# Performance work log

Measured on AMD Instinct MI355X. Metric: run time of the kernel, lower is better.

The kernel has to match this reference:

```python
import jax, jax.numpy as jnp
import numpy as np

B, S, H, NH = 2, 2048, 2048, 32
HD = H // NH  # 64

def _causal_mask(b, s, dtype=jnp.float32):
    neg = jnp.finfo(dtype).min
    m = jnp.where(jnp.tril(jnp.ones((s, s), dtype=bool)), 0.0, neg).astype(dtype)
    return jnp.broadcast_to(m[None, None], (b, 1, s, s))

def setup_inputs() -> dict:
    key = jax.random.key(0)
    k1, k2, k3, k4, k5 = jax.random.split(key, 5)
    scale = 1.0 / np.sqrt(H)
    return {
        "hidden_states": jax.random.normal(k1, (B, S, H), jnp.float32),
        "attention_mask": _causal_mask(B, S),
        "Wq": jax.random.normal(k2, (H, H), jnp.float32) * scale,
        "Wk": jax.random.normal(k3, (H, H), jnp.float32) * scale,
        "Wv": jax.random.normal(k4, (H, H), jnp.float32) * scale,
        "Wo": jax.random.normal(k5, (H, H), jnp.float32) * scale,
    }

def reference(hidden_states, attention_mask, Wq, Wk, Wv, Wo):
    b, s, _ = hidden_states.shape
    dt = hidden_states.dtype
    def proj(W):  # torch Linear: x @ W.T -> [b, nh, s, hd]
        return (hidden_states @ W.T).reshape(b, s, NH, HD).transpose(0, 2, 1, 3)
    q, k, v = proj(Wq), proj(Wk), proj(Wv)
    attn = jnp.einsum('bhqd,bhkd->bhqk', q, k) / np.sqrt(HD)
    attn = attn + attention_mask
    attn = jnp.maximum(attn, jnp.finfo(attn.dtype).min)
    attn = jax.nn.softmax(attn.astype(jnp.float32), axis=-1).astype(dt)
    out = jnp.einsum('bhqk,bhkd->bhqd', attn, v)
    out = out.transpose(0, 2, 1, 3).reshape(b, s, H)
    return out @ Wo.T
```

## Files before the change

kernel.cpp:

```cpp
#include <hip/hip_runtime.h>
#include <hip/hip_bf16.h>
#include <stdint.h>

#define S_LEN 2048
#define NHEAD 32
#define HDIM  64

using bf16x8 = __attribute__((ext_vector_type(8))) short;
using f32x4  = __attribute__((ext_vector_type(4))) float;
using f32x16 = __attribute__((ext_vector_type(16))) float;

__device__ __forceinline__ uint16_t f2bf(float f) {
  union { float f; uint32_t u; } c; c.f = f;
  uint32_t u = c.u;
  return (uint16_t)((u + 0x7FFFu + ((u >> 16) & 1u)) >> 16);
}

__device__ __forceinline__ void load_lds16(const void* g, void* l) {
  __builtin_amdgcn_global_load_lds(
      (const __attribute__((address_space(1))) void*)g,
      (__attribute__((address_space(3))) void*)l, 16, 0, 0);
}

__device__ __forceinline__ f32x16 mfma32(bf16x8 a, bf16x8 b, f32x16 c) {
  return __builtin_amdgcn_mfma_f32_32x32x16_bf16(a, b, c, 0, 0, 0);
}

__device__ __forceinline__ uint32_t cvtpk(float lo, float hi_) {
  uint32_t d;
  asm("v_cvt_pk_bf16_f32 %0, %1, %2" : "=v"(d) : "v"(lo), "v"(hi_));
  return d;
}
__device__ __forceinline__ void plswap(uint32_t& a, uint32_t& b) {
  asm volatile("v_permlane32_swap_b32 %0, %1" : "+v"(a), "+v"(b));
}
__device__ __forceinline__ float exp2_hw(float x) {
  float r;
  asm("v_exp_f32 %0, %1" : "=v"(r) : "v"(x));
  return r;
}

__global__ __launch_bounds__(256) void conv_batch(
    const float* __restrict__ X, const float* __restrict__ Wq,
    const float* __restrict__ Wk, const float* __restrict__ Wv,
    const float* __restrict__ Wo, uint16_t* __restrict__ Xbf,
    uint16_t* __restrict__ Wqk, uint16_t* __restrict__ Wvb,
    uint16_t* __restrict__ Wob) {
  int i = blockIdx.x * 256 + threadIdx.x;
  const float* src; uint16_t* dst; int o;
  if (i < 2097152)      { src = X;  dst = Xbf;           o = i; }
  else if (i < 3145728) { src = Wq; dst = Wqk;           o = i - 2097152; }
  else if (i < 4194304) { src = Wk; dst = Wqk + 4194304; o = i - 3145728; }
  else if (i < 5242880) { src = Wv; dst = Wvb;           o = i - 4194304; }
  else                  { src = Wo; dst = Wob;           o = i - 5242880; }
  float4 v = ((const float4*)src)[o];
  uint64_t packed = (uint64_t)f2bf(v.x) | ((uint64_t)f2bf(v.y) << 16) |
                    ((uint64_t)f2bf(v.z) << 32) | ((uint64_t)f2bf(v.w) << 48);
  ((uint64_t*)dst)[o] = packed;
}

__global__ __launch_bounds__(512, 2) void gemm_qk(
    const uint16_t* __restrict__ A, const uint16_t* __restrict__ Bw,
    uint16_t* __restrict__ Qo, uint16_t* __restrict__ Ko, float qscale) {
  extern __shared__ char smem[];
  const int t = threadIdx.x;
  const int lane = t & 63, w = t >> 6;
  const int lrow = lane & 15, lgrp = lane >> 4;
  const int wr = w >> 2, wc = w & 3;
  const int id = blockIdx.x;
  const int swz = (id & 7) * 32 + (id >> 3);
  const int bm = (swz & 15) * 256, bn = (swz >> 4) * 256;
  constexpr int NT = 2048 / 64;

  const f32x4 zero4 = {0.f, 0.f, 0.f, 0.f};
  f32x4 acc[8][4];
#pragma unroll
  for (int mi = 0; mi < 8; ++mi)
#pragma unroll
    for (int ni = 0; ni < 4; ++ni) acc[mi][ni] = zero4;

  auto stage_half = [&](const uint16_t* __restrict__ G, int grow0,
                        char* dstHalf, int kt) {
#pragma unroll
    for (int j = 0; j < 2; ++j) {
      const int s = t + j * 512;
      const int lr = s >> 3;
      const int sc = (s & 7) ^ (lr & 7);
      load_lds16(G + (size_t)(grow0 + lr) * 2048 + kt * 64 + sc * 8,
                 dstHalf + j * 8192 + w * 1024);
    }
  };
  auto ldA = [&](const char* bufA, int mh, int mi2, int kk) -> bf16x8 {
    const int lr = mh * 64 + mi2 * 16 + lrow;
    const int c = kk * 4 + lgrp;
    return *(const bf16x8*)(bufA + wr * 16384 + lr * 128 +
                            ((c ^ (lr & 7)) << 4));
  };
  auto ldB = [&](const char* bufB, int nh, int ni2, int kk) -> bf16x8 {
    const int lr = (wc & 1) * 64 + nh * 32 + ni2 * 16 + lrow;
    const int c = kk * 4 + lgrp;
    return *(const bf16x8*)(bufB + (wc >> 1) * 16384 + lr * 128 +
                            ((c ^ (lr & 7)) << 4));
  };

  stage_half(A, bm, smem, 0);
  stage_half(A, bm + 128, smem + 16384, 0);
  stage_half(Bw, bn, smem + 32768, 0);
  stage_half(Bw, bn + 128, smem + 49152, 0);

  for (int kt = 0; kt < NT; ++kt) {
    char* bufc = smem + (kt & 1) * 65536;
    char* bufn = smem + ((kt + 1) & 1) * 65536;
    const char* Ac = bufc;
    const char* Bc = bufc + 32768;
    const bool pre = (kt + 1 < NT);

    asm volatile("s_waitcnt vmcnt(0)" ::: "memory");
    __builtin_amdgcn_s_barrier();

    bf16x8 aF[4][2], b0[2][2], b1[2][2];

#pragma unroll
    for (int mi2 = 0; mi2 < 4; ++mi2)
#pragma unroll
      for (int kk = 0; kk < 2; ++kk) aF[mi2][kk] = ldA(Ac, 0, mi2, kk);
#pragma unroll
    for (int ni2 = 0; ni2 < 2; ++ni2)
#pragma unroll
      for (int kk = 0; kk < 2; ++kk) b0[ni2][kk] = ldB(Bc, 0, ni2, kk);
    if (pre) stage_half(A, bm, bufn, kt + 1);
    asm volatile("s_waitcnt lgkmcnt(0)" ::: "memory");
    __builtin_amdgcn_sched_barrier(0);
    __builtin_amdgcn_s_setprio(1);
#pragma unroll
    for (int mi2 = 0; mi2 < 4; ++mi2)
#pragma unroll
      for (int ni2 = 0; ni2 < 2; ++ni2)
#pragma unroll
        for (int kk = 0; kk < 2; ++kk)
          acc[mi2][ni2] = __builtin_amdgcn_mfma_f32_16x16x32_bf16(
              aF[mi2][kk], b0[ni2][kk], acc[mi2][ni2], 0, 0, 0);
    __builtin_amdgcn_s_setprio(0);

#pragma unroll
    for (int ni2 = 0; ni2 < 2; ++ni2)
#pragma unroll
      for (int kk = 0; kk < 2; ++kk) b1[ni2][kk] = ldB(Bc, 1, ni2, kk);
    if (pre) stage_half(A, bm + 128, bufn + 16384, kt + 1);
    asm volatile("s_waitcnt lgkmcnt(0)" ::: "memory");
    __builtin_amdgcn_sched_barrier(0);
    __builtin_amdgcn_s_setprio(1);
#pragma unroll
    for (int mi2 = 0; mi2 < 4; ++mi2)
#pragma unroll
      for (int ni2 = 0; ni2 < 2; ++ni2)
#pragma unroll
        for (int kk = 0; kk < 2; ++kk)
          acc[mi2][2 + ni2] = __builtin_amdgcn_mfma_f32_16x16x32_bf16(
              aF[mi2][kk], b1[ni2][kk], acc[mi2][2 + ni2], 0, 0, 0);
    __builtin_amdgcn_s_setprio(0);

#pragma unroll
    for (int mi2 = 0; mi2 < 4; ++mi2)
#pragma unroll
      for (int kk = 0; kk < 2; ++kk) aF[mi2][kk] = ldA(Ac, 1, mi2, kk);
    if (pre) stage_half(Bw, bn, bufn + 32768, kt + 1);
    asm volatile("s_waitcnt lgkmcnt(0)" ::: "memory");
    __builtin_amdgcn_sched_barrier(0);
    __builtin_amdgcn_s_setprio(1);
#pragma unroll
    for (int mi2 = 0; mi2 < 4; ++mi2)
#pragma unroll
      for (int ni2 = 0; ni2 < 2; ++ni2)
#pragma unroll
        for (int kk = 0; kk < 2; ++kk)
          acc[4 + mi2][2 + ni2] = __builtin_amdgcn_mfma_f32_16x16x32_bf16(
              aF[mi2][kk], b1[ni2][kk], acc[4 + mi2][2 + ni2], 0, 0, 0);
    __builtin_amdgcn_s_setprio(0);

    if (pre) stage_half(Bw, bn + 128, bufn + 49152, kt + 1);
    __builtin_amdgcn_s_setprio(1);
#pragma unroll
    for (int mi2 = 0; mi2 < 4; ++mi2)
#pragma unroll
      for (int ni2 = 0; ni2 < 2; ++ni2)
#pragma unroll
        for (int kk = 0; kk < 2; ++kk)
          acc[4 + mi2][ni2] = __builtin_amdgcn_mfma_f32_16x16x32_bf16(
              aF[mi2][kk], b0[ni2][kk], acc[4 + mi2][ni2], 0, 0, 0);
    __builtin_amdgcn_s_setprio(0);
  }

  const bool isQ = (bn < 2048);
#pragma unroll
  for (int mi = 0; mi < 8; ++mi) {
#pragma unroll
    for (int ni = 0; ni < 4; ++ni) {
      const int n = bn + wc * 64 + ni * 16 + lrow;
      const int n2 = isQ ? n : (n - 2048);
      const int h = n2 >> 6, d = n2 & 63;
#pragma unroll
      for (int r = 0; r < 4; ++r) {
        const int m = bm + wr * 128 + mi * 16 + lgrp * 4 + r;
        const int b = m >> 11, s = m & 2047;
        const size_t off = (((size_t)(b * NHEAD + h) * S_LEN + s) * HDIM) + d;
        if (isQ) Qo[off] = f2bf(acc[mi][ni][r] * qscale);
        else     Ko[off] = f2bf(acc[mi][ni][r]);
      }
    }
  }
}

template<int MODE>
__global__ __launch_bounds__(256, 3) void gemm_nt(
    const uint16_t* __restrict__ A, const uint16_t* __restrict__ B,
    void* __restrict__ C, int M, int N, int K, float scale) {
  __shared__ __align__(16) char smem[3][16384];

  const int t = threadIdx.x;
  const int lane = t & 63, w = t >> 6;
  const int lrow = lane & 15, lgrp = lane >> 4;
  const int bm = blockIdx.y * 128, bn = blockIdx.x * 128;
  const int wm = (w >> 1) * 64, wn = (w & 1) * 64;
  const int NT = K / 32;

  const f32x4 zero4 = {0.f, 0.f, 0.f, 0.f};
  f32x4 acc[4][4];
#pragma unroll
  for (int mi = 0; mi < 4; ++mi)
#pragma unroll
    for (int ni = 0; ni < 4; ++ni) acc[mi][ni] = zero4;

  auto stage_mat = [&](const uint16_t* __restrict__ G, int grow0,
                       char* ldsbase, int kt) {
#pragma unroll
    for (int j = 0; j < 2; ++j) {
      const int s = t + j * 256;
      const int row = s >> 2;
      const int sc = (s & 3) ^ ((row >> 1) & 3);
      load_lds16(G + (size_t)(grow0 + row) * K + kt + sc * 8,
                 ldsbase + j * 4096 + w * 1024);
    }
  };
  auto ldf = [&](const char* Mb, int base, int i) -> bf16x8 {
    const int row = base + i * 16 + lrow;
    return *(const bf16x8*)(Mb + row * 64 + ((lgrp ^ ((row >> 1) & 3)) << 4));
  };

  stage_mat(A, bm, smem[0], 0);
  stage_mat(B, bn, smem[0] + 8192, 0);
  stage_mat(A, bm, smem[1], 32);
  stage_mat(B, bn, smem[1] + 8192, 32);

  for (int kt = 0; kt < NT; ++kt) {
    char* cur = smem[kt % 3];
    if (kt < NT - 1) asm volatile("s_waitcnt vmcnt(4)" ::: "memory");
    else             asm volatile("s_waitcnt vmcnt(0)" ::: "memory");
    __builtin_amdgcn_s_barrier();

    if (kt + 2 < NT) {
      char* nx2 = smem[(kt + 2) % 3];
      stage_mat(A, bm, nx2, (kt + 2) * 32);
      stage_mat(B, bn, nx2 + 8192, (kt + 2) * 32);
    }

    bf16x8 aF[4], bF[4];
#pragma unroll
    for (int mi = 0; mi < 4; ++mi) aF[mi] = ldf(cur, wm, mi);
#pragma unroll
    for (int ni = 0; ni < 4; ++ni) bF[ni] = ldf(cur + 8192, wn, ni);
#pragma unroll
    for (int mi = 0; mi < 4; ++mi)
#pragma unroll
      for (int ni = 0; ni < 4; ++ni)
        acc[mi][ni] = __builtin_amdgcn_mfma_f32_16x16x32_bf16(
            aF[mi], bF[ni], acc[mi][ni], 0, 0, 0);
  }

#pragma unroll
  for (int mi = 0; mi < 4; ++mi) {
#pragma unroll
    for (int ni = 0; ni < 4; ++ni) {
      const int n = bn + wn + ni * 16 + lrow;
#pragma unroll
      for (int r = 0; r < 4; ++r) {
        const int m = bm + wm + mi * 16 + lgrp * 4 + r;
        const float v = acc[mi][ni][r] * scale;
        if (MODE == 2) {
          ((float*)C)[(size_t)m * N + n] = v;
        } else {
          const int h = m >> 6, d = m & 63;
          const int b = n >> 11, s = n & 2047;
          ((uint16_t*)C)[(((size_t)(b * NHEAD + h) * HDIM + d) * S_LEN) + s] =
              f2bf(v);
        }
      }
    }
  }
}

__global__ __launch_bounds__(256, 2) void attn_kernel(
    const uint16_t* __restrict__ Q, const uint16_t* __restrict__ K,
    const uint16_t* __restrict__ Vt, uint16_t* __restrict__ O) {
  extern __shared__ __align__(16) char asmem[];
  const int t = threadIdx.x, lane = t & 63, w = t >> 6;
  const int qcol = lane & 31, hi = lane >> 5;
  const int id = blockIdx.x;
  const int bh = (id & 7) * 8 + ((id >> 3) & 7);
  const int p = id >> 6;
  const int b = bh >> 5, h = bh & 31;

  const uint16_t* Qbh = Q + (size_t)bh * S_LEN * HDIM;
  const uint16_t* Kbh = K + (size_t)bh * S_LEN * HDIM;
  const uint16_t* Vbh = Vt + (size_t)bh * HDIM * S_LEN;

  const int srow = lane >> 3;
  const int schunk = (lane & 7) ^ srow;

  const short one_bf = (short)0x3F80;
  const bf16x8 onesf = {one_bf, one_bf, one_bf, one_bf,
                        one_bf, one_bf, one_bf, one_bf};

  auto Kbuf = [&](int bi, int sub) -> char* {
    return asmem + (bi * 2 + sub) * 8192;
  };
  auto Vbuf = [&](int bi, int sub) -> char* {
    return asmem + 32768 + (bi * 2 + sub) * 8192;
  };

  auto stage = [&](int k0, int bi) {
#pragma unroll
    for (int sub = 0; sub < 2; ++sub) {
      const int kb = k0 + sub * 64;
#pragma unroll
      for (int j = 0; j < 2; ++j) {
        const int r = j * 32 + w * 8 + srow;
        load_lds16(Kbh + (size_t)(kb + r) * HDIM + schunk * 8,
                   Kbuf(bi, sub) + j * 4096 + w * 1024);
        load_lds16(Vbh + (size_t)r * S_LEN + kb + schunk * 8,
                   Vbuf(bi, sub) + j * 4096 + w * 1024);
      }
    }
  };

  const int rk0 = qcol, rk1 = 32 + qcol;
  const int x0 = qcol & 7;

  for (int pass = 0; pass < 2; ++pass) {
    const int jq = pass ? (15 - p) : p;
    const int qw = jq * 128 + w * 32;
    const int qg = qw + qcol;

    bf16x8 qB[4];
    {
      const uint16_t* qp = Qbh + (size_t)qg * HDIM + hi * 8;
#pragma unroll
      for (int j = 0; j < 4; ++j) qB[j] = *(const bf16x8*)(qp + 16 * j);
    }

    f32x16 oacc0, oacc1, oS;
#pragma unroll
    for (int r = 0; r < 16; ++r) { oacc0[r] = 0.f; oacc1[r] = 0.f; oS[r] = 0.f; }

    auto qk = [&](const char* Kc, f32x16& s0, f32x16& s1) {
#pragma unroll
      for (int r = 0; r < 16; ++r) { s0[r] = 0.f; s1[r] = 0.f; }
      __builtin_amdgcn_s_setprio(1);
#pragma unroll
      for (int j = 0; j < 4; ++j) {
        bf16x8 kf0 = *(const bf16x8*)(Kc + rk0 * 128 + (((2*j+hi) ^ x0) << 4));
        bf16x8 kf1 = *(const bf16x8*)(Kc + rk1 * 128 + (((2*j+hi) ^ x0) << 4));
        s0 = mfma32(kf0, qB[j], s0);
        s1 = mfma32(kf1, qB[j], s1);
      }
      __builtin_amdgcn_s_setprio(0);
    };
    auto smx = [&](int k0s, f32x16& s0, f32x16& s1) {
      if (k0s + 63 > qw) {
#pragma unroll
        for (int r = 0; r < 16; ++r) {
          const int krow = (r & 3) + 8 * (r >> 2) + 4 * hi;
          s0[r] = (k0s + krow <= qg) ? exp2_hw(s0[r]) : 0.f;
          s1[r] = (k0s + 32 + krow <= qg) ? exp2_hw(s1[r]) : 0.f;
        }
      } else {
#pragma unroll
        for (int r = 0; r < 16; ++r) {
          s0[r] = exp2_hw(s0[r]);
          s1[r] = exp2_hw(s1[r]);
        }
      }
    };
    auto repack = [&](const f32x16& s0, const f32x16& s1, bf16x8 (&paf)[4]) {
#pragma unroll
      for (int tt = 0; tt < 4; ++tt) {
        const int o = 8 * (tt & 1);
        uint32_t a0, a1, a2, a3;
        if (tt < 2) {
          a0 = cvtpk(s0[o + 0], s0[o + 1]);
          a1 = cvtpk(s0[o + 2], s0[o + 3]);
          a2 = cvtpk(s0[o + 4], s0[o + 5]);
          a3 = cvtpk(s0[o + 6], s0[o + 7]);
        } else {
          a0 = cvtpk(s1[o + 0], s1[o + 1]);
          a1 = cvtpk(s1[o + 2], s1[o + 3]);
          a2 = cvtpk(s1[o + 4], s1[o + 5]);
          a3 = cvtpk(s1[o + 6], s1[o + 7]);
        }
        plswap(a0, a2);
        plswap(a1, a3);
        union { uint32_t u[4]; bf16x8 v; } pk;
        pk.u[0] = a0; pk.u[1] = a1; pk.u[2] = a2; pk.u[3] = a3;
        paf[tt] = pk.v;
      }
    };
    auto pv = [&](const char* Vc, const bf16x8 (&paf)[4]) {
      __builtin_amdgcn_s_setprio(1);
#pragma unroll
      for (int tt = 0; tt < 4; ++tt) {
        const int c = 2 * tt + hi;
        bf16x8 v0f = *(const bf16x8*)(Vc + rk0 * 128 + ((c ^ x0) << 4));
        bf16x8 v1f = *(const bf16x8*)(Vc + rk1 * 128 + ((c ^ x0) << 4));
        oacc0 = mfma32(paf[tt], v0f, oacc0);
        oacc1 = mfma32(paf[tt], v1f, oacc1);
        oS = mfma32(paf[tt], onesf, oS);
      }
      __builtin_amdgcn_s_setprio(0);
    };

    const int nt = jq + 1;
    for (int kt = 0; kt < nt; ++kt) {
      const int cur = kt & 1;
      const int k0 = kt * 128;
      if (kt == 0) { __syncthreads(); stage(0, 0); }
      __syncthreads();
      if (kt + 1 < nt) stage((kt + 1) * 128, cur ^ 1);

      const bool a1 = (k0 + 64 <= qw + 31);
      f32x16 s0a, s1a, s0b, s1b;
      qk(Kbuf(cur, 0), s0a, s1a);
      if (a1) qk(Kbuf(cur, 1), s0b, s1b);
      smx(k0, s0a, s1a);
      bf16x8 paf[4];
      repack(s0a, s1a, paf);
      pv(Vbuf(cur, 0), paf);
      if (a1) {
        smx(k0 + 64, s0b, s1b);
        repack(s0b, s1b, paf);
        pv(Vbuf(cur, 1), paf);
      }
    }

#pragma unroll
    for (int r = 0; r < 16; ++r) {
      const int qrow = (r & 3) + 8 * (r >> 2) + 4 * hi;
      const float inv = 1.0f / oS[r];
      const size_t base = ((size_t)b * S_LEN + qw + qrow) * 2048 + h * 64;
      O[base + qcol] = f2bf(oacc0[r] * inv);
      O[base + 32 + qcol] = f2bf(oacc1[r] * inv);
    }
  }
}

extern "C" void kernel_launch(void* const* d_in, const int* in_sizes, int n_in,
                              void* d_out, int out_size, void* d_ws,
                              size_t ws_size, hipStream_t stream) {
  const float* X  = (const float*)d_in[0];
  const float* Wq = (const float*)d_in[2];
  const float* Wk = (const float*)d_in[3];
  const float* Wv = (const float*)d_in[4];
  const float* Wo = (const float*)d_in[5];
  float* out = (float*)d_out;

  char* ws = (char*)d_ws;
  uint16_t* Xbf = (uint16_t*)ws;
  uint16_t* Wqk = (uint16_t*)(ws + 16777216);
  uint16_t* Qb  = (uint16_t*)(ws + 33554432);
  uint16_t* Kb  = (uint16_t*)(ws + 50331648);
  uint16_t* Wsm = (uint16_t*)(ws + 67108864);
  uint16_t* Wob = (uint16_t*)(ws + 75497472);
  uint16_t* Vtb = Wqk;
  uint16_t* Ob  = Xbf;

  const float qscale = 0.125f * 1.4426950408889634f;

  hipFuncSetAttribute((const void*)gemm_qk,
                      hipFuncAttributeMaxDynamicSharedMemorySize, 131072);
  hipFuncSetAttribute((const void*)attn_kernel,
                      hipFuncAttributeMaxDynamicSharedMemorySize, 65536);

  conv_batch<<<24576, 256, 0, stream>>>(X, Wq, Wk, Wv, Wo, Xbf, Wqk, Wsm, Wob);
  gemm_qk<<<256, 512, 131072, stream>>>(Xbf, Wqk, Qb, Kb, qscale);
  gemm_nt<1><<<dim3(32, 16), 256, 0, stream>>>(Wsm, Xbf, Vtb, 2048, 4096, 2048, 1.0f);
  attn_kernel<<<512, 256, 65536, stream>>>(Qb, Kb, Vtb, Ob);
  gemm_nt<2><<<dim3(16, 32), 256, 0, stream>>>(Ob, Wob, out, 4096, 2048, 2048, 1.0f);
}
```

Measured before the change: 215.5 us.

## Restructure gemm_nt to K=64 tiles with double buffering and interleaved prefetch

Changes the generic NT GEMM from a triple-buffered K=32 pipeline to a double-buffered K=64 pipeline with an 8-way XOR swizzle. Each iteration splits into two K=32 halves and issues the next A and B global-to-LDS loads between them, with priority bumps around the MFMA blocks. This halves the number of barriers per K and aims to overlap loads with compute. The cost is double the LDS per block (64KB) and lower declared occupancy (2 blocks/CU), and the wait now drains all loads before each tile.

```diff
diff --git a/kernel.cpp b/kernel.cpp
--- a/kernel.cpp
+++ b/kernel.cpp
@@ -212,17 +212,17 @@
 }
 
 template<int MODE>
-__global__ __launch_bounds__(256, 3) void gemm_nt(
+__global__ __launch_bounds__(256, 2) void gemm_nt(
     const uint16_t* __restrict__ A, const uint16_t* __restrict__ B,
     void* __restrict__ C, int M, int N, int K, float scale) {
-  __shared__ __align__(16) char smem[3][16384];
+  __shared__ __align__(16) char smem[2][32768];
 
   const int t = threadIdx.x;
   const int lane = t & 63, w = t >> 6;
   const int lrow = lane & 15, lgrp = lane >> 4;
   const int bm = blockIdx.y * 128, bn = blockIdx.x * 128;
   const int wm = (w >> 1) * 64, wn = (w & 1) * 64;
-  const int NT = K / 32;
+  const int NT = K / 64;
 
   const f32x4 zero4 = {0.f, 0.f, 0.f, 0.f};
   f32x4 acc[4][4];
@@ -232,49 +232,65 @@
     for (int ni = 0; ni < 4; ++ni) acc[mi][ni] = zero4;
 
   auto stage_mat = [&](const uint16_t* __restrict__ G, int grow0,
-                       char* ldsbase, int kt) {
-#pragma unroll
-    for (int j = 0; j < 2; ++j) {
+                       char* dst, int kt) {
+#pragma unroll
+    for (int j = 0; j < 4; ++j) {
       const int s = t + j * 256;
-      const int row = s >> 2;
-      const int sc = (s & 3) ^ ((row >> 1) & 3);
-      load_lds16(G + (size_t)(grow0 + row) * K + kt + sc * 8,
-                 ldsbase + j * 4096 + w * 1024);
-    }
-  };
-  auto ldf = [&](const char* Mb, int base, int i) -> bf16x8 {
+      const int lr = s >> 3;
+      const int sc = (s & 7) ^ (lr & 7);
+      load_lds16(G + (size_t)(grow0 + lr) * K + kt * 64 + sc * 8,
+                 dst + j * 4096 + w * 1024);
+    }
+  };
+  auto ldf = [&](const char* Mb, int base, int i, int kk) -> bf16x8 {
     const int row = base + i * 16 + lrow;
-    return *(const bf16x8*)(Mb + row * 64 + ((lgrp ^ ((row >> 1) & 3)) << 4));
+    const int c = kk * 4 + lgrp;
+    return *(const bf16x8*)(Mb + row * 128 + ((c ^ (row & 7)) << 4));
   };
 
   stage_mat(A, bm, smem[0], 0);
-  stage_mat(B, bn, smem[0] + 8192, 0);
-  stage_mat(A, bm, smem[1], 32);
-  stage_mat(B, bn, smem[1] + 8192, 32);
+  stage_mat(B, bn, smem[0] + 16384, 0);
 
   for (int kt = 0; kt < NT; ++kt) {
-    char* cur = smem[kt % 3];
-    if (kt < NT - 1) asm volatile("s_waitcnt vmcnt(4)" ::: "memory");
-    else             asm volatile("s_waitcnt vmcnt(0)" ::: "memory");
+    char* bufc = smem[kt & 1];
+    char* bufn = smem[(kt + 1) & 1];
+    const bool pre = (kt + 1 < NT);
+
+    asm volatile("s_waitcnt vmcnt(0)" ::: "memory");
     __builtin_amdgcn_s_barrier();
 
-    if (kt + 2 < NT) {
-      char* nx2 = smem[(kt + 2) % 3];
-      stage_mat(A, bm, nx2, (kt + 2) * 32);
-      stage_mat(B, bn, nx2 + 8192, (kt + 2) * 32);
-    }
-
     bf16x8 aF[4], bF[4];
 #pragma unroll
-    for (int mi = 0; mi < 4; ++mi) aF[mi] = ldf(cur, wm, mi);
-#pragma unroll
-    for (int ni = 0; ni < 4; ++ni) bF[ni] = ldf(cur + 8192, wn, ni);
+    for (int mi = 0; mi < 4; ++mi) aF[mi] = ldf(bufc, wm, mi, 0);
+#pragma unroll
+    for (int ni = 0; ni < 4; ++ni) bF[ni] = ldf(bufc + 16384, wn, ni, 0);
+    if (pre) stage_mat(A, bm, bufn, kt + 1);
+    asm volatile("s_waitcnt lgkmcnt(0)" ::: "memory");
+    __builtin_amdgcn_sched_barrier(0);
+    __builtin_amdgcn_s_setprio(1);
 #pragma unroll
     for (int mi = 0; mi < 4; ++mi)
 #pragma unroll
       for (int ni = 0; ni < 4; ++ni)
         acc[mi][ni] = __builtin_amdgcn_mfma_f32_16x16x32_bf16(
             aF[mi], bF[ni], acc[mi][ni], 0, 0, 0);
+    __builtin_amdgcn_s_setprio(0);
+
+#pragma unroll
+    for (int mi = 0; mi < 4; ++mi) aF[mi] = ldf(bufc, wm, mi, 1);
+#pragma unroll
+    for (int ni = 0; ni < 4; ++ni) bF[ni] = ldf(bufc + 16384, wn, ni, 1);
+    if (pre) stage_mat(B, bn, bufn + 16384, kt + 1);
+    asm volatile("s_waitcnt lgkmcnt(0)" ::: "memory");
+    __builtin_amdgcn_sched_barrier(0);
+    __builtin_amdgcn_s_setprio(1);
+#pragma unroll
+    for (int mi = 0; mi < 4; ++mi)
+#pragma unroll
+      for (int ni = 0; ni < 4; ++ni)
+        acc[mi][ni] = __builtin_amdgcn_mfma_f32_16x16x32_bf16(
+            aF[mi], bF[ni], acc[mi][ni], 0, 0, 0);
+    __builtin_amdgcn_s_setprio(0);
   }
 
 #pragma unroll
```

After: 205.2 us, median of 2. 4.8% less time.
